# Performance work log

Measured on AMD Instinct MI355X. Metric: run time of the kernel, lower is better.

The kernel has to match this reference:

```python
import jax, jax.numpy as jnp
import numpy as np
from math import ceil

TAU = 0.25  # diffusion step size (forward arg tau in the torch module)


def setup_inputs() -> dict:
    key = jax.random.key(0)
    ks = jax.random.split(key, 10)
    N, D_IN, H, C, E = 8192, 128, 64, 40, 262144
    s = 0.05
    return {
        "x_in": jax.random.normal(ks[0], (N, D_IN), dtype=jnp.float32),
        "enc_w": jax.random.normal(ks[1], (D_IN, H), dtype=jnp.float32) * s,
        "enc_b": jnp.zeros((H,), dtype=jnp.float32),
        "wk_w": jax.random.normal(ks[2], (H, H), dtype=jnp.float32) * s,
        "wk_b": jnp.zeros((H,), dtype=jnp.float32),
        "wq_w": jax.random.normal(ks[3], (H, H), dtype=jnp.float32) * s,
        "wq_b": jnp.zeros((H,), dtype=jnp.float32),
        "dec_w": jax.random.normal(ks[4], (H, C), dtype=jnp.float32) * s,
        "dec_b": jnp.zeros((C,), dtype=jnp.float32),
        "edges": jax.random.randint(ks[5], (E, 2), 0, N, dtype=jnp.int32),
        "T": 4,
    }


def reference(x_in, enc_w, enc_b, wk_w, wk_b, wq_w, wq_b, dec_w, dec_b, edges, T):
    N, _ = x_in.shape
    steps = int(ceil(T / TAU))

    # encoder
    x0 = x_in @ enc_w + enc_b                      # [N, H]
    H = x0.shape[1]

    # per-edge attention scores -> dense row-normalized matrix A (as in torch)
    kx = x0 @ wk_w + wk_b                          # [N, H]
    qx = x0 @ wq_w + wq_b                          # [N, H]
    u, v = edges[:, 0], edges[:, 1]
    scores = jnp.sum(kx[u] * qx[v], axis=-1) / H   # [E]
    A = jnp.zeros((N, N), dtype=x0.dtype).at[u, v].set(jnp.exp(scores))
    row_sums = A.sum(axis=1, keepdims=True)
    A = A / jnp.where(row_sums == 0, 1.0, row_sums)

    # diffusion: x_{k+1} = (I + tau*(A - I)) x_k, iterated ceil(T/tau) times
    U = jnp.eye(N, dtype=x0.dtype) + TAU * (A - jnp.eye(N, dtype=x0.dtype))

    def body(x_k, _):
        return U @ x_k, None

    x_final, _ = jax.lax.scan(body, x0, None, length=steps)

    # decoder
    return x_final @ dec_w + dec_b                 # [N, num_classes]
```

## Files before the change

kernel.cpp:

```cpp
#include <hip/hip_runtime.h>
#include <hip/hip_bf16.h>

constexpr int N_   = 8192;
constexpr int DIN_ = 128;
constexpr int H_   = 64;
constexpr int C_   = 40;
constexpr int STEPS_ = 16;
constexpr int CAP_ = 128;
#define TAU_ 0.25f

typedef float    f32x4 __attribute__((ext_vector_type(4)));
typedef unsigned int u32x4 __attribute__((ext_vector_type(4)));
typedef _Float16 f16x4 __attribute__((ext_vector_type(4)));

__device__ __forceinline__ unsigned int packvw(int v, float w)
{
    unsigned int u = __float_as_uint(w);
    u += 0x0FFFu + ((u >> 13) & 1u);
    u &= 0xFFFFE000u;
    return u | (unsigned int)v;
}

__global__ __launch_bounds__(256) void front_k(const float* __restrict__ xin,
    const float* __restrict__ ew, const float* __restrict__ eb,
    const float* __restrict__ wk, const float* __restrict__ kb,
    const float* __restrict__ wq, const float* __restrict__ qb,
    const float* __restrict__ dw,
    float* __restrict__ kx, float* __restrict__ qx,
    float* __restrict__ z0, _Float16* __restrict__ zh0)
{
    __shared__ float xs[16][64];
    int wloc = threadIdx.x >> 6;
    int lane = threadIdx.x & 63;
    int r0   = (blockIdx.x * 4 + wloc) * 4;

    const float* xr = xin + (size_t)r0 * DIN_;
    float bv = eb[lane];
    float a0 = bv, a1 = bv, a2 = bv, a3 = bv;
    for (int k = 0; k < DIN_; ++k) {
        float wv = ew[k * H_ + lane];
        a0 = fmaf(xr[k],            wv, a0);
        a1 = fmaf(xr[DIN_ + k],     wv, a1);
        a2 = fmaf(xr[2 * DIN_ + k], wv, a2);
        a3 = fmaf(xr[3 * DIN_ + k], wv, a3);
    }
    float* xls = &xs[wloc * 4][0];
    xls[lane] = a0; xls[64 + lane] = a1; xls[128 + lane] = a2; xls[192 + lane] = a3;

    float kbv = kb[lane], qbv = qb[lane];
    float ak0 = kbv, ak1 = kbv, ak2 = kbv, ak3 = kbv;
    float aq0 = qbv, aq1 = qbv, aq2 = qbv, aq3 = qbv;
    for (int k = 0; k < H_; ++k) {
        float wkv = wk[k * H_ + lane];
        float wqv = wq[k * H_ + lane];
        float x0v = xls[k], x1v = xls[64 + k], x2v = xls[128 + k], x3v = xls[192 + k];
        ak0 = fmaf(x0v, wkv, ak0);  aq0 = fmaf(x0v, wqv, aq0);
        ak1 = fmaf(x1v, wkv, ak1);  aq1 = fmaf(x1v, wqv, aq1);
        ak2 = fmaf(x2v, wkv, ak2);  aq2 = fmaf(x2v, wqv, aq2);
        ak3 = fmaf(x3v, wkv, ak3);  aq3 = fmaf(x3v, wqv, aq3);
    }
    float* ok = kx + (size_t)r0 * H_ + lane;
    float* oq = qx + (size_t)r0 * H_ + lane;
    ok[0] = ak0; ok[H_] = ak1; ok[2 * H_] = ak2; ok[3 * H_] = ak3;
    oq[0] = aq0; oq[H_] = aq1; oq[2 * H_] = aq2; oq[3 * H_] = aq3;

    if (lane < C_) {
        float z0a = 0.f, z1a = 0.f, z2a = 0.f, z3a = 0.f;
        for (int k = 0; k < H_; ++k) {
            float dv = dw[k * C_ + lane];
            z0a = fmaf(xls[k],       dv, z0a);
            z1a = fmaf(xls[64 + k],  dv, z1a);
            z2a = fmaf(xls[128 + k], dv, z2a);
            z3a = fmaf(xls[192 + k], dv, z3a);
        }
        z0[(size_t)r0 * C_ + lane]       = z0a;
        z0[(size_t)(r0 + 1) * C_ + lane] = z1a;
        z0[(size_t)(r0 + 2) * C_ + lane] = z2a;
        z0[(size_t)(r0 + 3) * C_ + lane] = z3a;
        zh0[(size_t)r0 * C_ + lane]       = (_Float16)z0a;
        zh0[(size_t)(r0 + 1) * C_ + lane] = (_Float16)z1a;
        zh0[(size_t)(r0 + 2) * C_ + lane] = (_Float16)z2a;
        zh0[(size_t)(r0 + 3) * C_ + lane] = (_Float16)z3a;
    }
}

__global__ __launch_bounds__(256) void score_place_k(const int2* __restrict__ edges,
    const float* __restrict__ kx, const float* __restrict__ qx,
    int* __restrict__ fill, int2* __restrict__ bvw, int E)
{
    int t  = blockIdx.x * 256 + threadIdx.x;
    int eg = t >> 3;
    int sl = t & 7;
    if (eg >= E) return;
    int2 uv = edges[eg];
    const float4* kr = (const float4*)(kx + (size_t)uv.x * H_);
    const float4* qr = (const float4*)(qx + (size_t)uv.y * H_);
    float4 a0 = kr[sl], a1 = kr[sl + 8];
    float4 b0 = qr[sl], b1 = qr[sl + 8];
    float d = a0.x * b0.x + a0.y * b0.y + a0.z * b0.z + a0.w * b0.w
            + a1.x * b1.x + a1.y * b1.y + a1.z * b1.z + a1.w * b1.w;
    d += __shfl_xor(d, 1);
    d += __shfl_xor(d, 2);
    d += __shfl_xor(d, 4);
    if (sl == 0) {
        float w = expf(d * (1.0f / (float)H_));
        int pos = atomicAdd(&fill[uv.x], 1);
        if (pos < CAP_)
            bvw[(size_t)uv.x * CAP_ + pos] = make_int2(uv.y, __float_as_int(w));
    }
}

__global__ __launch_bounds__(256) void dedup_k(const int* __restrict__ fill,
    const int2* __restrict__ bvw, unsigned int* __restrict__ pw,
    int* __restrict__ nc)
{
    __shared__ unsigned int bm[4][256];
    int wv   = threadIdx.x >> 6;
    int lane = threadIdx.x & 63;
    int row  = blockIdx.x * 4 + wv;
    unsigned int* b = bm[wv];
    for (int i = lane; i < 256; i += 64) b[i] = 0;
    __syncthreads();
    int f = fill[row];
    if (f > CAP_) f = CAP_;
    int padded = (f + 15) & ~15;
    size_t base = (size_t)row * CAP_;
    int2 ea = make_int2(0, 0), eb = make_int2(0, 0);
    float wa = 0.f, wb = 0.f;
    if (lane < f) {
        ea = bvw[base + lane];
        unsigned int m = 1u << (ea.x & 31);
        unsigned int old = atomicOr(&b[ea.x >> 5], m);
        wa = (old & m) ? 0.0f : __int_as_float(ea.y);
    }
    if (64 + lane < f) {
        eb = bvw[base + 64 + lane];
        unsigned int m = 1u << (eb.x & 31);
        unsigned int old = atomicOr(&b[eb.x >> 5], m);
        wb = (old & m) ? 0.0f : __int_as_float(eb.y);
    }
    float wsum = wa + wb;
    #pragma unroll
    for (int off = 1; off < 64; off <<= 1) wsum += __shfl_xor(wsum, off);
    if (lane == 0) nc[row] = padded >> 4;
    if (f == 0) return;
    float scale = TAU_ / wsum;
    int pa = lane;
    int na = (pa & ~15) | ((pa & 3) << 2) | ((pa & 15) >> 2);
    int pb = 64 + lane;
    int nb = (pb & ~15) | ((pb & 3) << 2) | ((pb & 15) >> 2);
    if (pa < padded) pw[base + na] = packvw(ea.x, wa * scale);
    if (pb < padded) pw[base + nb] = packvw(eb.x, wb * scale);
}

template <bool LAST>
__global__ __launch_bounds__(256) void stepz_k(const float* __restrict__ zin,
    const _Float16* __restrict__ zhin, float* __restrict__ zout,
    _Float16* __restrict__ zhout, const int* __restrict__ nc,
    const unsigned int* __restrict__ pw, const float* __restrict__ db)
{
    int row  = (blockIdx.x * 256 + threadIdx.x) >> 6;
    int lane = threadIdx.x & 63;
    int grp  = lane >> 4;
    int col4 = lane & 15;
    int c9   = (col4 < 10) ? col4 : 9;
    int ch   = c9 << 2;
    int ncv  = nc[row];
    const unsigned int* pwrow = pw + (size_t)row * CAP_ + (grp << 2);
    f32x4 acc = {0.f, 0.f, 0.f, 0.f};
    u32x4 q = *(const u32x4*)pwrow;
    for (int c = 0; c < ncv; ++c) {
        f16x4 h0 = *(const f16x4*)(zhin + (size_t)(q[0] & 0x1FFFu) * C_ + ch);
        f16x4 h1 = *(const f16x4*)(zhin + (size_t)(q[1] & 0x1FFFu) * C_ + ch);
        f16x4 h2 = *(const f16x4*)(zhin + (size_t)(q[2] & 0x1FFFu) * C_ + ch);
        f16x4 h3 = *(const f16x4*)(zhin + (size_t)(q[3] & 0x1FFFu) * C_ + ch);
        int cn = (c + 1 < ncv) ? (c + 1) : c;
        u32x4 qn = *(const u32x4*)(pwrow + ((size_t)cn << 4));
        float w0 = __uint_as_float(q[0] & 0xFFFFE000u);
        float w1 = __uint_as_float(q[1] & 0xFFFFE000u);
        float w2 = __uint_as_float(q[2] & 0xFFFFE000u);
        float w3 = __uint_as_float(q[3] & 0xFFFFE000u);
        acc[0] = fmaf(w0, (float)h0[0], acc[0]); acc[1] = fmaf(w0, (float)h0[1], acc[1]);
        acc[2] = fmaf(w0, (float)h0[2], acc[2]); acc[3] = fmaf(w0, (float)h0[3], acc[3]);
        acc[0] = fmaf(w1, (float)h1[0], acc[0]); acc[1] = fmaf(w1, (float)h1[1], acc[1]);
        acc[2] = fmaf(w1, (float)h1[2], acc[2]); acc[3] = fmaf(w1, (float)h1[3], acc[3]);
        acc[0] = fmaf(w2, (float)h2[0], acc[0]); acc[1] = fmaf(w2, (float)h2[1], acc[1]);
        acc[2] = fmaf(w2, (float)h2[2], acc[2]); acc[3] = fmaf(w2, (float)h2[3], acc[3]);
        acc[0] = fmaf(w3, (float)h3[0], acc[0]); acc[1] = fmaf(w3, (float)h3[1], acc[1]);
        acc[2] = fmaf(w3, (float)h3[2], acc[2]); acc[3] = fmaf(w3, (float)h3[3], acc[3]);
        q = qn;
    }
    acc[0] += __shfl_xor(acc[0], 16); acc[1] += __shfl_xor(acc[1], 16);
    acc[2] += __shfl_xor(acc[2], 16); acc[3] += __shfl_xor(acc[3], 16);
    acc[0] += __shfl_xor(acc[0], 32); acc[1] += __shfl_xor(acc[1], 32);
    acc[2] += __shfl_xor(acc[2], 32); acc[3] += __shfl_xor(acc[3], 32);
    if (grp == 0 && col4 < 10) {
        f32x4 xr = *(const f32x4*)(zin + (size_t)row * C_ + (col4 << 2));
        f32x4 r;
        r[0] = fmaf(1.0f - TAU_, xr[0], acc[0]);
        r[1] = fmaf(1.0f - TAU_, xr[1], acc[1]);
        r[2] = fmaf(1.0f - TAU_, xr[2], acc[2]);
        r[3] = fmaf(1.0f - TAU_, xr[3], acc[3]);
        if (LAST) {
            f32x4 bb = *(const f32x4*)(db + (col4 << 2));
            r[0] += bb[0]; r[1] += bb[1]; r[2] += bb[2]; r[3] += bb[3];
        }
        *(f32x4*)(zout + (size_t)row * C_ + (col4 << 2)) = r;
        if (!LAST) {
            f16x4 rh;
            rh[0] = (_Float16)r[0]; rh[1] = (_Float16)r[1];
            rh[2] = (_Float16)r[2]; rh[3] = (_Float16)r[3];
            *(f16x4*)(zhout + (size_t)row * C_ + (col4 << 2)) = rh;
        }
    }
}

extern "C" void kernel_launch(void* const* d_in, const int* in_sizes, int n_in,
                              void* d_out, int out_size, void* d_ws, size_t ws_size,
                              hipStream_t stream)
{
    const float* x_in  = (const float*)d_in[0];
    const float* enc_w = (const float*)d_in[1];
    const float* enc_b = (const float*)d_in[2];
    const float* wk_w  = (const float*)d_in[3];
    const float* wk_b  = (const float*)d_in[4];
    const float* wq_w  = (const float*)d_in[5];
    const float* wq_b  = (const float*)d_in[6];
    const float* dec_w = (const float*)d_in[7];
    const float* dec_b = (const float*)d_in[8];
    const int2*  edges = (const int2*)d_in[9];
    const int E = in_sizes[9] / 2;
    float* out = (float*)d_out;

    char* ws = (char*)d_ws;
    float*        za   = (float*)(ws + 0);
    float*        zb   = (float*)(ws + (2u << 20));
    float*        kx   = (float*)(ws + (4u << 20));
    float*        qx   = (float*)(ws + (6u << 20));
    int2*         bvw  = (int2*) (ws + (8u << 20));
    unsigned int* pw   = (unsigned int*)(ws + (16u << 20));
    int*          fill = (int*)  (ws + (20u << 20));
    int*          nc   = (int*)  (ws + (20u << 20) + (64u << 10));
    _Float16*     zha  = (_Float16*)(ws + (21u << 20));
    _Float16*     zhb  = (_Float16*)(ws + (22u << 20));

    hipMemsetAsync(fill, 0, N_ * sizeof(int), stream);

    front_k<<<N_ / 16, 256, 0, stream>>>(x_in, enc_w, enc_b, wk_w, wk_b,
                                         wq_w, wq_b, dec_w, kx, qx, za, zha);
    score_place_k<<<(E * 8 + 255) / 256, 256, 0, stream>>>(edges, kx, qx, fill, bvw, E);
    dedup_k<<<N_ / 4, 256, 0, stream>>>(fill, bvw, pw, nc);

    float*    zi  = za;
    _Float16* zhi = zha;
    for (int s = 0; s < STEPS_ - 1; ++s) {
        float*    zo  = (zi == za) ? zb : za;
        _Float16* zho = (zhi == zha) ? zhb : zha;
        stepz_k<false><<<N_ / 4, 256, 0, stream>>>(zi, zhi, zo, zho, nc, pw, dec_b);
        zi = zo; zhi = zho;
    }
    stepz_k<true><<<N_ / 4, 256, 0, stream>>>(zi, zhi, out, nullptr, nc, pw, dec_b);
}
```

Before: 153.2 us.

## Compact per-row edge lists into CSR layout via prefix-sum scan

Adds a single-block scan kernel that prefix-sums the padded per-row edge counts. The packed edge entries are then written contiguously (CSR-style) instead of at fixed 128-entry row strides, and the step kernels read each row's offset and count from one int2. This shrinks the packed-weight footprint (about 32 entries per row on average instead of 128 slots), improving cache locality across the 16 diffusion steps. The cost is an extra serial single-block kernel launch, and the workspace offsets are reshuffled.

```diff
diff --git a/kernel.cpp b/kernel.cpp
--- a/kernel.cpp
+++ b/kernel.cpp
@@ -110,9 +110,39 @@
     }
 }
 
+__global__ __launch_bounds__(256) void scan_k(const int* __restrict__ fill,
+    int2* __restrict__ rinfo)
+{
+    __shared__ int partial[256];
+    int t = threadIdx.x;
+    const int chunk = N_ / 256;
+    int base = t * chunk;
+    int s = 0;
+    for (int i = 0; i < chunk; ++i) {
+        int f = fill[base + i];
+        if (f > CAP_) f = CAP_;
+        s += (f + 15) & ~15;
+    }
+    partial[t] = s;
+    __syncthreads();
+    if (t == 0) {
+        int run = 0;
+        for (int i = 0; i < 256; ++i) { int tmp = partial[i]; partial[i] = run; run += tmp; }
+    }
+    __syncthreads();
+    int run = partial[t];
+    for (int i = 0; i < chunk; ++i) {
+        int f = fill[base + i];
+        if (f > CAP_) f = CAP_;
+        int padded = (f + 15) & ~15;
+        rinfo[base + i] = make_int2(run, padded >> 4);
+        run += padded;
+    }
+}
+
 __global__ __launch_bounds__(256) void dedup_k(const int* __restrict__ fill,
-    const int2* __restrict__ bvw, unsigned int* __restrict__ pw,
-    int* __restrict__ nc)
+    const int2* __restrict__ rinfo, const int2* __restrict__ bvw,
+    unsigned int* __restrict__ pw)
 {
     __shared__ unsigned int bm[4][256];
     int wv   = threadIdx.x >> 6;
@@ -124,17 +154,18 @@
     int f = fill[row];
     if (f > CAP_) f = CAP_;
     int padded = (f + 15) & ~15;
-    size_t base = (size_t)row * CAP_;
+    size_t src = (size_t)row * CAP_;
+    size_t dst = (size_t)rinfo[row].x;
     int2 ea = make_int2(0, 0), eb = make_int2(0, 0);
     float wa = 0.f, wb = 0.f;
     if (lane < f) {
-        ea = bvw[base + lane];
+        ea = bvw[src + lane];
         unsigned int m = 1u << (ea.x & 31);
         unsigned int old = atomicOr(&b[ea.x >> 5], m);
         wa = (old & m) ? 0.0f : __int_as_float(ea.y);
     }
     if (64 + lane < f) {
-        eb = bvw[base + 64 + lane];
+        eb = bvw[src + 64 + lane];
         unsigned int m = 1u << (eb.x & 31);
         unsigned int old = atomicOr(&b[eb.x >> 5], m);
         wb = (old & m) ? 0.0f : __int_as_float(eb.y);
@@ -142,21 +173,20 @@
     float wsum = wa + wb;
     #pragma unroll
     for (int off = 1; off < 64; off <<= 1) wsum += __shfl_xor(wsum, off);
-    if (lane == 0) nc[row] = padded >> 4;
     if (f == 0) return;
     float scale = TAU_ / wsum;
     int pa = lane;
     int na = (pa & ~15) | ((pa & 3) << 2) | ((pa & 15) >> 2);
     int pb = 64 + lane;
     int nb = (pb & ~15) | ((pb & 3) << 2) | ((pb & 15) >> 2);
-    if (pa < padded) pw[base + na] = packvw(ea.x, wa * scale);
-    if (pb < padded) pw[base + nb] = packvw(eb.x, wb * scale);
+    if (pa < padded) pw[dst + na] = packvw(ea.x, wa * scale);
+    if (pb < padded) pw[dst + nb] = packvw(eb.x, wb * scale);
 }
 
 template <bool LAST>
 __global__ __launch_bounds__(256) void stepz_k(const float* __restrict__ zin,
     const _Float16* __restrict__ zhin, float* __restrict__ zout,
-    _Float16* __restrict__ zhout, const int* __restrict__ nc,
+    _Float16* __restrict__ zhout, const int2* __restrict__ rinfo,
     const unsigned int* __restrict__ pw, const float* __restrict__ db)
 {
     int row  = (blockIdx.x * 256 + threadIdx.x) >> 6;
@@ -165,8 +195,9 @@
     int col4 = lane & 15;
     int c9   = (col4 < 10) ? col4 : 9;
     int ch   = c9 << 2;
-    int ncv  = nc[row];
-    const unsigned int* pwrow = pw + (size_t)row * CAP_ + (grp << 2);
+    int2 ri  = rinfo[row];
+    int ncv  = ri.y;
+    const unsigned int* pwrow = pw + (size_t)ri.x + (grp << 2);
     f32x4 acc = {0.f, 0.f, 0.f, 0.f};
     u32x4 q = *(const u32x4*)pwrow;
     for (int c = 0; c < ncv; ++c) {
@@ -239,25 +270,26 @@
     float*        qx   = (float*)(ws + (6u << 20));
     int2*         bvw  = (int2*) (ws + (8u << 20));
     unsigned int* pw   = (unsigned int*)(ws + (16u << 20));
-    int*          fill = (int*)  (ws + (20u << 20));
-    int*          nc   = (int*)  (ws + (20u << 20) + (64u << 10));
-    _Float16*     zha  = (_Float16*)(ws + (21u << 20));
-    _Float16*     zhb  = (_Float16*)(ws + (22u << 20));
+    int*          fill = (int*)  (ws + (18u << 20));
+    int2*         rinfo= (int2*) (ws + (18u << 20) + (64u << 10));
+    _Float16*     zha  = (_Float16*)(ws + (19u << 20));
+    _Float16*     zhb  = (_Float16*)(ws + (20u << 20));
 
     hipMemsetAsync(fill, 0, N_ * sizeof(int), stream);
 
     front_k<<<N_ / 16, 256, 0, stream>>>(x_in, enc_w, enc_b, wk_w, wk_b,
                                          wq_w, wq_b, dec_w, kx, qx, za, zha);
     score_place_k<<<(E * 8 + 255) / 256, 256, 0, stream>>>(edges, kx, qx, fill, bvw, E);
-    dedup_k<<<N_ / 4, 256, 0, stream>>>(fill, bvw, pw, nc);
+    scan_k<<<1, 256, 0, stream>>>(fill, rinfo);
+    dedup_k<<<N_ / 4, 256, 0, stream>>>(fill, rinfo, bvw, pw);
 
     float*    zi  = za;
     _Float16* zhi = zha;
     for (int s = 0; s < STEPS_ - 1; ++s) {
         float*    zo  = (zi == za) ? zb : za;
         _Float16* zho = (zhi == zha) ? zhb : zha;
-        stepz_k<false><<<N_ / 4, 256, 0, stream>>>(zi, zhi, zo, zho, nc, pw, dec_b);
+        stepz_k<false><<<N_ / 4, 256, 0, stream>>>(zi, zhi, zo, zho, rinfo, pw, dec_b);
         zi = zo; zhi = zho;
     }
-    stepz_k<true><<<N_ / 4, 256, 0, stream>>>(zi, zhi, out, nullptr, nc, pw, dec_b);
-}
+    stepz_k<true><<<N_ / 4, 256, 0, stream>>>(zi, zhi, out, nullptr, rinfo, pw, dec_b);
+}
```

New measurement: 161.1 us. +5.1%, slower.
